# Performance work log

Measured on AMD Instinct MI355X. Metric: run time of the kernel, lower is better.

The kernel has to match this reference:

```python
import jax, jax.numpy as jnp
import numpy as np

GROUPSIZE = 128
# 6 possible 2:4 sparsity patterns (choose 2 nonzeros out of each group of 4 rows)
_PATTERNS = jnp.array([
    [1, 1, 0, 0], [1, 0, 1, 0], [1, 0, 0, 1],
    [0, 1, 1, 0], [0, 1, 0, 1], [0, 0, 1, 1],
], dtype=jnp.float32)


def setup_inputs() -> dict:
    key = jax.random.key(0)
    k1, k2, k3, k4 = jax.random.split(key, 4)
    M, K, N = 4096, 4096, 8192
    x = jax.random.normal(k1, (M, K), dtype=jnp.float16)
    # int4 codes in [0, 15] (stored unpacked; bit-packing is layout-only)
    qweight = jax.random.randint(k2, (K, N), 0, 16, dtype=jnp.int32)
    # 2:4 pattern index per group of 4 consecutive K rows
    meta = jax.random.randint(k3, (K // 4, N), 0, 6, dtype=jnp.int32)
    # positive group scales, typical quantization magnitude
    scale = (jax.random.uniform(k4, (K // GROUPSIZE, N), dtype=jnp.float32) * 0.02 + 0.005).astype(jnp.float16)
    return {"x": x, "qweight": qweweight_fix(qweight), "meta": meta, "scale": scale}


def qweweight_fix(q):
    return q  # identity; kept for clarity


def _dequant(qweight, meta, scale):
    """Dequantize int4 2:4-sparse weights with group scales -> dense fp32 [K, N]."""
    K, N = qweight.shape
    mask = _PATTERNS[meta]                      # [K//4, N, 4]
    mask = jnp.transpose(mask, (0, 2, 1)).reshape(K, N)  # [K, N]
    s = jnp.repeat(scale.astype(jnp.float32), GROUPSIZE, axis=0)  # [K, N]
    # symmetric int4: zero-point = 8 (maxq+1)//2
    return (qweight.astype(jnp.float32) - 8.0) * mask * s


def reference(x, qweight, meta, scale):
    W = _dequant(qweight, meta, scale)          # [K, N] fp32
    out = x.astype(jnp.float32) @ W             # fp32 accumulation, as in the kernel
    return out.astype(x.dtype)                  # [M, N] fp16
```

## Files before the change

kernel.cpp:

```cpp
#include <hip/hip_runtime.h>
#include <cmath>


typedef __attribute__((ext_vector_type(8))) short bf16x8;
typedef __attribute__((ext_vector_type(4))) float f32x4;

__device__ inline unsigned short f2bf(float f) {
    union { float f; unsigned u; } v; v.f = f;
    unsigned r = (v.u + 0x7FFFu + ((v.u >> 16) & 1u)) >> 16;
    return (unsigned short)r;
}

__global__ __launch_bounds__(256) void convert_x(
    const float* __restrict__ x, unsigned short* __restrict__ xb, long long total)
{
    const long long base = ((long long)blockIdx.x * 256 + threadIdx.x) * 8;
    if (base + 8 > total) return;
    const float4 a = *reinterpret_cast<const float4*>(x + base);
    const float4 b = *reinterpret_cast<const float4*>(x + base + 4);
    uint4 o;
    o.x = (unsigned)f2bf(a.x) | ((unsigned)f2bf(a.y) << 16);
    o.y = (unsigned)f2bf(a.z) | ((unsigned)f2bf(a.w) << 16);
    o.z = (unsigned)f2bf(b.x) | ((unsigned)f2bf(b.y) << 16);
    o.w = (unsigned)f2bf(b.z) | ((unsigned)f2bf(b.w) << 16);
    *reinterpret_cast<uint4*>(xb + base) = o;
}

__global__ __launch_bounds__(256) void dequant_wt(
    const int* __restrict__ q, const int* __restrict__ meta,
    const float* __restrict__ scale,
    unsigned short* __restrict__ wt,
    int K, int N, int nbase)
{
    __shared__ __align__(16) unsigned short lds[64 * 68];
    const int t  = threadIdx.x;
    const int n  = t & 63;
    const int kc = t >> 6;
    const int k0 = blockIdx.x * 64;
    const int nl0 = blockIdx.y * 64;
    const int ng = nbase + nl0 + n;
    const int g = k0 >> 7;
    const float sc = scale[(size_t)g * N + ng];
    const unsigned lut = 0xCA6953u;

    #pragma unroll
    for (int p = 0; p < 4; ++p) {
        const int kl = p * 16 + kc * 4;
        const int kg = k0 + kl;
        const int mv = meta[(size_t)(kg >> 2) * N + ng];
        const unsigned pat = (lut >> (mv * 4)) & 0xFu;
        unsigned short w[4];
        #pragma unroll
        for (int j = 0; j < 4; ++j) {
            const int qv = q[(size_t)(kg + j) * N + ng];
            const float wf = ((pat >> j) & 1u) ? (float)(qv - 8) * sc : 0.0f;
            w[j] = f2bf(wf);
        }
        uint2 pk;
        pk.x = (unsigned)w[0] | ((unsigned)w[1] << 16);
        pk.y = (unsigned)w[2] | ((unsigned)w[3] << 16);
        *reinterpret_cast<uint2*>(&lds[n * 68 + kl]) = pk;
    }
    __syncthreads();
    #pragma unroll
    for (int p = 0; p < 2; ++p) {
        const int idx = p * 256 + t;
        const int nr  = idx >> 3;
        const int ch  = idx & 7;
        const uint2 lo = *reinterpret_cast<const uint2*>(&lds[nr * 68 + ch * 8]);
        const uint2 hi = *reinterpret_cast<const uint2*>(&lds[nr * 68 + ch * 8 + 4]);
        uint4 vv; vv.x = lo.x; vv.y = lo.y; vv.z = hi.x; vv.w = hi.y;
        *reinterpret_cast<uint4*>(&wt[(size_t)(nl0 + nr) * K + k0 + ch * 8]) = vv;
    }
}

#define BAR() do { asm volatile("" ::: "memory"); \
                   __builtin_amdgcn_s_barrier(); \
                   asm volatile("" ::: "memory"); } while (0)

#define GLDS(g, s) __builtin_amdgcn_global_load_lds( \
    (const __attribute__((address_space(1))) void*)(g), \
    (__attribute__((address_space(3))) void*)(s), 16, 0, 0)

#define MFMA(d, x, y) d = __builtin_amdgcn_mfma_f32_16x16x32_bf16(x, y, d, 0, 0, 0)

__global__ __launch_bounds__(512, 2) void gemm256(
    const unsigned short* __restrict__ A,
    const unsigned short* __restrict__ Bt,
    float* __restrict__ C,
    int M, int N, int K, int nbase)
{
    __shared__ __align__(16) unsigned short As[32768];
    __shared__ __align__(16) unsigned short Bs[32768];

    const int t    = threadIdx.x;
    const int w    = t >> 6;
    const int lane = t & 63;
    const int wm   = w >> 2;
    const int wn   = w & 3;
    const int l16  = lane & 15;
    const int quad = lane >> 4;

    const int gx = gridDim.x;
    int bid = blockIdx.y * gx + blockIdx.x;
    const int nwg = gx * gridDim.y;
    if (nwg >= 8) {
        const int q8 = nwg >> 3, r8 = nwg & 7;
        const int xcd = bid & 7, off = bid >> 3;
        bid = (xcd < r8 ? xcd * (q8 + 1) : r8 * (q8 + 1) + (xcd - r8) * q8) + off;
    }
    const int n0 = (bid % gx) * 256;
    const int m0 = (bid / gx) * 256;

    const int    csrc = ((lane & 7) ^ ((lane >> 3) & 7)) * 8;
    const size_t aB = (size_t)(m0 + w * 8 + (lane >> 3)) * K + csrc;
    const size_t bB = (size_t)(n0 + w * 8 + (lane >> 3)) * K + csrc;
    const size_t J  = (size_t)64 * K;
    const size_t H  = (size_t)128 * K;
    const int sdst  = w * 512;

    const int sw0 = ((quad ^ (lane & 7)) * 8);
    const int sw1 = (((4 + quad) ^ (lane & 7)) * 8);
    const int aR  = wm * 8192 + l16 * 64;
    const int bR  = (wn >> 1) * 8192 + ((wn & 1) * 64 + l16) * 64;

    int kA = 0, kB = 0;

#define STAGE_A(buf, h) do { \
    GLDS(A + aB + (size_t)(h) * H + kA, &As[(buf)*16384 + (h)*8192 + sdst]); \
    GLDS(A + aB + (size_t)(h) * H + J + kA, &As[(buf)*16384 + (h)*8192 + 4096 + sdst]); \
  } while (0)
#define STAGE_B(buf, h) do { \
    GLDS(Bt + bB + (size_t)(h) * H + kB, &Bs[(buf)*16384 + (h)*8192 + sdst]); \
    GLDS(Bt + bB + (size_t)(h) * H + J + kB, &Bs[(buf)*16384 + (h)*8192 + 4096 + sdst]); \
  } while (0)

    f32x4 acc[8][4];
    #pragma unroll
    for (int i = 0; i < 8; ++i)
        #pragma unroll
        for (int j = 0; j < 4; ++j)
            acc[i][j] = (f32x4){0.f, 0.f, 0.f, 0.f};

    STAGE_B(0, 0); STAGE_B(0, 1); kB += 64;
    STAGE_A(0, 0); STAGE_A(0, 1); kA += 64;
    STAGE_B(1, 0); STAGE_B(1, 1); kB += 64;
    asm volatile("s_waitcnt vmcnt(4)" ::: "memory");
    BAR();

    bf16x8 a[4][2], b0[2][2], b1[2][2];

#define PHASES(buf, obuf) do { \
   \
  _Pragma("unroll") for (int i = 0; i < 4; ++i) { \
    a[i][0] = *(const bf16x8*)&As[(buf)*16384 + aR + i*1024 + sw0]; \
    a[i][1] = *(const bf16x8*)&As[(buf)*16384 + aR + i*1024 + sw1]; } \
  _Pragma("unroll") for (int j = 0; j < 2; ++j) { \
    b0[j][0] = *(const bf16x8*)&Bs[(buf)*16384 + bR + j*1024 + sw0]; \
    b0[j][1] = *(const bf16x8*)&Bs[(buf)*16384 + bR + j*1024 + sw1]; } \
  STAGE_A(obuf, 0); \
  BAR(); \
  asm volatile("s_waitcnt lgkmcnt(0)" ::: "memory"); \
  __builtin_amdgcn_s_setprio(1); \
  _Pragma("unroll") for (int i = 0; i < 4; ++i) \
    _Pragma("unroll") for (int j = 0; j < 2; ++j) { \
      MFMA(acc[i][j], a[i][0], b0[j][0]); MFMA(acc[i][j], a[i][1], b0[j][1]); } \
  __builtin_amdgcn_s_setprio(0); \
  BAR(); \
   \
  _Pragma("unroll") for (int j = 0; j < 2; ++j) { \
    b1[j][0] = *(const bf16x8*)&Bs[(buf)*16384 + bR + (2+j)*1024 + sw0]; \
    b1[j][1] = *(const bf16x8*)&Bs[(buf)*16384 + bR + (2+j)*1024 + sw1]; } \
  STAGE_A(obuf, 1); kA += 64; if (kA >= K) kA = 0; \
  BAR(); \
  asm volatile("s_waitcnt lgkmcnt(0)" ::: "memory"); \
  __builtin_amdgcn_s_setprio(1); \
  _Pragma("unroll") for (int i = 0; i < 4; ++i) \
    _Pragma("unroll") for (int j = 0; j < 2; ++j) { \
      MFMA(acc[i][2+j], a[i][0], b1[j][0]); MFMA(acc[i][2+j], a[i][1], b1[j][1]); } \
  __builtin_amdgcn_s_setprio(0); \
  BAR(); \
   \
  _Pragma("unroll") for (int i = 0; i < 4; ++i) { \
    a[i][0] = *(const bf16x8*)&As[(buf)*16384 + aR + (4+i)*1024 + sw0]; \
    a[i][1] = *(const bf16x8*)&As[(buf)*16384 + aR + (4+i)*1024 + sw1]; } \
  STAGE_B(buf, 0); \
  BAR(); \
  asm volatile("s_waitcnt lgkmcnt(0)" ::: "memory"); \
  __builtin_amdgcn_s_setprio(1); \
  _Pragma("unroll") for (int i = 0; i < 4; ++i) \
    _Pragma("unroll") for (int j = 0; j < 2; ++j) { \
      MFMA(acc[4+i][2+j], a[i][0], b1[j][0]); MFMA(acc[4+i][2+j], a[i][1], b1[j][1]); } \
  __builtin_amdgcn_s_setprio(0); \
  BAR(); \
   \
  STAGE_B(buf, 1); kB += 64; if (kB >= K) kB = 0; \
  BAR(); \
  __builtin_amdgcn_s_setprio(1); \
  _Pragma("unroll") for (int i = 0; i < 4; ++i) \
    _Pragma("unroll") for (int j = 0; j < 2; ++j) { \
      MFMA(acc[4+i][j], a[i][0], b0[j][0]); MFMA(acc[4+i][j], a[i][1], b0[j][1]); } \
  __builtin_amdgcn_s_setprio(0); \
  asm volatile("s_waitcnt vmcnt(4)" ::: "memory"); \
  BAR(); \
} while (0)

    const int NIT = K >> 7;
    for (int it = 0; it < NIT; ++it) {
        PHASES(0, 1);
        PHASES(1, 0);
    }

    asm volatile("s_waitcnt vmcnt(0)" ::: "memory");

    const int mBase = m0 + wm * 128;
    const int nBase = nbase + n0 + wn * 64;
    #pragma unroll
    for (int i = 0; i < 8; ++i) {
        const int mrow = mBase + i * 16 + quad * 4;
        #pragma unroll
        for (int j = 0; j < 4; ++j) {
            const int ncol = nBase + j * 16 + l16;
            #pragma unroll
            for (int r = 0; r < 4; ++r)
                C[(size_t)(mrow + r) * N + ncol] = acc[i][j][r];
        }
    }
#undef STAGE_A
#undef STAGE_B
#undef PHASES
}

extern "C" void kernel_launch(void* const* d_in, const int* in_sizes, int n_in,
                              void* d_out, int out_size, void* d_ws, size_t ws_size,
                              hipStream_t stream)
{
    const float* x     = (const float*)d_in[0];
    const int*   q     = (const int*)d_in[1];
    const int*   meta  = (const int*)d_in[2];
    const float* scale = (const float*)d_in[3];
    float*       out   = (float*)d_out;

    const double s0 = (double)in_sizes[0];
    const double s1 = (double)in_sizes[1];
    const int K = (int)llround(sqrt(s0 * s1 / (double)out_size));
    const int M = in_sizes[0] / K;
    const int N = in_sizes[1] / K;

    unsigned short* xb = (unsigned short*)d_ws;
    const size_t xb_bytes = (size_t)M * (size_t)K * 2;
    unsigned short* wt = (unsigned short*)((char*)d_ws + xb_bytes);
    const size_t wt_avail = ws_size > xb_bytes ? ws_size - xb_bytes : 0;

    const long long total = (long long)M * K;
    convert_x<<<dim3((unsigned)((total / 8 + 255) / 256)), dim3(256), 0, stream>>>(
        x, xb, total);

    long long maxrows = (long long)(wt_avail / ((size_t)K * 2));
    int NC = (int)((maxrows / 256) * 256);
    if (NC > N) NC = N;
    if (NC < 256) NC = 256;

    for (int nbase = 0; nbase < N; nbase += NC) {
        const int nc = (N - nbase) < NC ? (N - nbase) : NC;
        dim3 g1(K / 64, nc / 64);
        dequant_wt<<<g1, dim3(256), 0, stream>>>(q, meta, scale, wt, K, N, nbase);
        dim3 g2(nc / 256, M / 256);
        gemm256<<<g2, dim3(512), 0, stream>>>(xb, wt, out, M, N, K, nbase);
    }
}
```

Measured before the change: 572.8 us.

## Prefetch next B fragment across phases and remap workgroups to XCD-local 2D tiles

Workgroups are now mapped so each XCD owns a contiguous 2D block of output tiles (half the M rows by a quarter of the N columns), replacing the flat round-robin XCD remap. The intent is better L2 reuse of A and B panels within each XCD. The main loop now ping-pongs two B register fragments, loading the first B fragment of the next buffer during the last phase of the current one. Both A stage loads are issued together at the start, with a new vmcnt(6) wait before the cross-buffer B read. The goal is fewer LDS-read stalls before the MFMA bursts, at the cost of extra registers and a wait-count ordering that has to stay correct.

```diff
diff --git a/kernel.cpp b/kernel.cpp
--- a/kernel.cpp
+++ b/kernel.cpp
@@ -101,16 +101,28 @@
     const int l16  = lane & 15;
     const int quad = lane >> 4;
 
-    const int gx = gridDim.x;
+    const int gx = gridDim.x, gy = gridDim.y;
     int bid = blockIdx.y * gx + blockIdx.x;
-    const int nwg = gx * gridDim.y;
-    if (nwg >= 8) {
-        const int q8 = nwg >> 3, r8 = nwg & 7;
-        const int xcd = bid & 7, off = bid >> 3;
-        bid = (xcd < r8 ? xcd * (q8 + 1) : r8 * (q8 + 1) + (xcd - r8) * q8) + off;
-    }
-    const int n0 = (bid % gx) * 256;
-    const int m0 = (bid / gx) * 256;
+    const int nwg = gx * gy;
+    int m0, n0;
+    if ((nwg & 7) == 0 && (gy & 1) == 0 && (gx & 3) == 0) {
+        const int xcd = bid & 7;
+        const int idx = bid >> 3;
+        const int cpr = gx >> 2;
+        const int lr  = idx / cpr;
+        const int lc  = idx - lr * cpr;
+        m0 = ((xcd >> 2) * (gy >> 1) + lr) * 256;
+        n0 = ((xcd & 3) * cpr + lc) * 256;
+    } else {
+        int b2 = bid;
+        if (nwg >= 8) {
+            const int q8 = nwg >> 3, r8 = nwg & 7;
+            const int xcd = bid & 7, off = bid >> 3;
+            b2 = (xcd < r8 ? xcd * (q8 + 1) : r8 * (q8 + 1) + (xcd - r8) * q8) + off;
+        }
+        n0 = (b2 % gx) * 256;
+        m0 = (b2 / gx) * 256;
+    }
 
     const int    csrc = ((lane & 7) ^ ((lane >> 3) & 7)) * 8;
     const size_t aB = (size_t)(m0 + w * 8 + (lane >> 3)) * K + csrc;
@@ -148,36 +160,38 @@
     asm volatile("s_waitcnt vmcnt(4)" ::: "memory");
     BAR();
 
-    bf16x8 a[4][2], b0[2][2], b1[2][2];
-
-#define PHASES(buf, obuf) do { \
+    bf16x8 a[4][2], bA_[2][2], bB_[2][2];
+
+    #pragma unroll
+    for (int j = 0; j < 2; ++j) {
+        bA_[j][0] = *(const bf16x8*)&Bs[bR + j * 1024 + sw0];
+        bA_[j][1] = *(const bf16x8*)&Bs[bR + j * 1024 + sw1];
+    }
+
+#define PHASES(buf, obuf, bcur, bnxt) do { \
    \
   _Pragma("unroll") for (int i = 0; i < 4; ++i) { \
     a[i][0] = *(const bf16x8*)&As[(buf)*16384 + aR + i*1024 + sw0]; \
     a[i][1] = *(const bf16x8*)&As[(buf)*16384 + aR + i*1024 + sw1]; } \
+  STAGE_A(obuf, 0); STAGE_A(obuf, 1); kA += 64; if (kA >= K) kA = 0; \
+  BAR(); \
+  asm volatile("s_waitcnt lgkmcnt(0)" ::: "memory"); \
+  __builtin_amdgcn_s_setprio(1); \
+  _Pragma("unroll") for (int i = 0; i < 4; ++i) \
+    _Pragma("unroll") for (int j = 0; j < 2; ++j) { \
+      MFMA(acc[i][j], a[i][0], bcur[j][0]); MFMA(acc[i][j], a[i][1], bcur[j][1]); } \
+  __builtin_amdgcn_s_setprio(0); \
+  BAR(); \
+   \
   _Pragma("unroll") for (int j = 0; j < 2; ++j) { \
-    b0[j][0] = *(const bf16x8*)&Bs[(buf)*16384 + bR + j*1024 + sw0]; \
-    b0[j][1] = *(const bf16x8*)&Bs[(buf)*16384 + bR + j*1024 + sw1]; } \
-  STAGE_A(obuf, 0); \
-  BAR(); \
-  asm volatile("s_waitcnt lgkmcnt(0)" ::: "memory"); \
-  __builtin_amdgcn_s_setprio(1); \
-  _Pragma("unroll") for (int i = 0; i < 4; ++i) \
-    _Pragma("unroll") for (int j = 0; j < 2; ++j) { \
-      MFMA(acc[i][j], a[i][0], b0[j][0]); MFMA(acc[i][j], a[i][1], b0[j][1]); } \
-  __builtin_amdgcn_s_setprio(0); \
-  BAR(); \
-   \
-  _Pragma("unroll") for (int j = 0; j < 2; ++j) { \
-    b1[j][0] = *(const bf16x8*)&Bs[(buf)*16384 + bR + (2+j)*1024 + sw0]; \
-    b1[j][1] = *(const bf16x8*)&Bs[(buf)*16384 + bR + (2+j)*1024 + sw1]; } \
-  STAGE_A(obuf, 1); kA += 64; if (kA >= K) kA = 0; \
-  BAR(); \
-  asm volatile("s_waitcnt lgkmcnt(0)" ::: "memory"); \
-  __builtin_amdgcn_s_setprio(1); \
-  _Pragma("unroll") for (int i = 0; i < 4; ++i) \
-    _Pragma("unroll") for (int j = 0; j < 2; ++j) { \
-      MFMA(acc[i][2+j], a[i][0], b1[j][0]); MFMA(acc[i][2+j], a[i][1], b1[j][1]); } \
+    bnxt[j][0] = *(const bf16x8*)&Bs[(buf)*16384 + bR + (2+j)*1024 + sw0]; \
+    bnxt[j][1] = *(const bf16x8*)&Bs[(buf)*16384 + bR + (2+j)*1024 + sw1]; } \
+  BAR(); \
+  asm volatile("s_waitcnt lgkmcnt(0)" ::: "memory"); \
+  __builtin_amdgcn_s_setprio(1); \
+  _Pragma("unroll") for (int i = 0; i < 4; ++i) \
+    _Pragma("unroll") for (int j = 0; j < 2; ++j) { \
+      MFMA(acc[i][2+j], a[i][0], bnxt[j][0]); MFMA(acc[i][2+j], a[i][1], bnxt[j][1]); } \
   __builtin_amdgcn_s_setprio(0); \
   BAR(); \
    \
@@ -190,16 +204,22 @@
   __builtin_amdgcn_s_setprio(1); \
   _Pragma("unroll") for (int i = 0; i < 4; ++i) \
     _Pragma("unroll") for (int j = 0; j < 2; ++j) { \
-      MFMA(acc[4+i][2+j], a[i][0], b1[j][0]); MFMA(acc[4+i][2+j], a[i][1], b1[j][1]); } \
-  __builtin_amdgcn_s_setprio(0); \
-  BAR(); \
-   \
+      MFMA(acc[4+i][2+j], a[i][0], bnxt[j][0]); MFMA(acc[4+i][2+j], a[i][1], bnxt[j][1]); } \
+  __builtin_amdgcn_s_setprio(0); \
+  BAR(); \
+   \
+   \
+  asm volatile("s_waitcnt vmcnt(6)" ::: "memory"); \
+  _Pragma("unroll") for (int j = 0; j < 2; ++j) { \
+    bnxt[j][0] = *(const bf16x8*)&Bs[(obuf)*16384 + bR + j*1024 + sw0]; \
+    bnxt[j][1] = *(const bf16x8*)&Bs[(obuf)*16384 + bR + j*1024 + sw1]; } \
   STAGE_B(buf, 1); kB += 64; if (kB >= K) kB = 0; \
   BAR(); \
-  __builtin_amdgcn_s_setprio(1); \
-  _Pragma("unroll") for (int i = 0; i < 4; ++i) \
-    _Pragma("unroll") for (int j = 0; j < 2; ++j) { \
-      MFMA(acc[4+i][j], a[i][0], b0[j][0]); MFMA(acc[4+i][j], a[i][1], b0[j][1]); } \
+  asm volatile("s_waitcnt lgkmcnt(0)" ::: "memory"); \
+  __builtin_amdgcn_s_setprio(1); \
+  _Pragma("unroll") for (int i = 0; i < 4; ++i) \
+    _Pragma("unroll") for (int j = 0; j < 2; ++j) { \
+      MFMA(acc[4+i][j], a[i][0], bcur[j][0]); MFMA(acc[4+i][j], a[i][1], bcur[j][1]); } \
   __builtin_amdgcn_s_setprio(0); \
   asm volatile("s_waitcnt vmcnt(4)" ::: "memory"); \
   BAR(); \
@@ -207,8 +227,8 @@
 
     const int NIT = K >> 7;
     for (int it = 0; it < NIT; ++it) {
-        PHASES(0, 1);
-        PHASES(1, 0);
+        PHASES(0, 1, bA_, bB_);
+        PHASES(1, 0, bB_, bA_);
     }
 
     asm volatile("s_waitcnt vmcnt(0)" ::: "memory");
```

Result: faster. 560.9 us (-2.1%).
